# Kernel optimization log

Hardware: AMD Instinct MI355X
Metric: run time of the kernel (lower is better)

Reference implementation:

```python
import jax, jax.numpy as jnp
import numpy as np

NEG_SLOPE = 0.2
LN_EPS = 1e-6

B, L, D, H = 32, 512, 256, 4
N = B * L
E = 65536
C = D  # per-head out channels (GATConv out_channels=d_model)


def setup_inputs() -> dict:
    key = jax.random.key(0)
    ks = jax.random.split(key, 10)
    s = 1.0 / np.sqrt(D)
    inputs = jax.random.normal(ks[0], (B, L, D), dtype=jnp.float32)
    edge_index = jax.random.randint(ks[1], (2, E), 0, N, dtype=jnp.int64)
    return {
        "inputs": inputs,
        "edge_index": edge_index,
        "ln_gamma": jnp.ones((D,), jnp.float32),
        "ln_beta": jnp.zeros((D,), jnp.float32),
        "W1": jax.random.normal(ks[2], (D, D), jnp.float32) * s,   # linear_before_gnn
        "b1": jnp.zeros((D,), jnp.float32),
        "W_gat": jax.random.normal(ks[3], (H * C, D), jnp.float32) * s,  # GATConv.lin (no bias)
        "att_src": jax.random.normal(ks[4], (H, C), jnp.float32) * s,
        "att_dst": jax.random.normal(ks[5], (H, C), jnp.float32) * s,
        "bias_gat": jnp.zeros((C,), jnp.float32),  # concat=False -> size out_channels
        "W2": jax.random.normal(ks[6], (D, D), jnp.float32) * s,   # linear_after_gnn
        "b2": jnp.zeros((D,), jnp.float32),
    }


def _gat_conv(x, edge_index, W_gat, att_src, att_dst, bias_gat):
    # x: [N, D] -> project to [N, H, C]
    xh = (x @ W_gat.T).reshape(N, H, C)
    # add self loops (PyG default add_self_loops=True)
    loops = jnp.arange(N, dtype=edge_index.dtype)
    src = jnp.concatenate([edge_index[0], loops])  # message source j
    dst = jnp.concatenate([edge_index[1], loops])  # message target i
    # per-node attention logits [N, H]
    a_src = jnp.einsum("nhc,hc->nh", xh, att_src)
    a_dst = jnp.einsum("nhc,hc->nh", xh, att_dst)
    # per-edge logits and segment softmax over destination node
    e = jax.nn.leaky_relu(a_src[src] + a_dst[dst], NEG_SLOPE)  # [Etot, H]
    e_max = jax.ops.segment_max(e, dst, num_segments=N)        # every node has a self loop
    e = jnp.exp(e - e_max[dst])
    denom = jax.ops.segment_sum(e, dst, num_segments=N)
    alpha = e / denom[dst]                                     # [Etot, H]
    # weighted message aggregation (dropout on alpha skipped: eval mode)
    msg = xh[src] * alpha[:, :, None]                          # [Etot, H, C]
    out = jax.ops.segment_sum(msg, dst, num_segments=N)        # [N, H, C]
    return out.mean(axis=1) + bias_gat                         # concat=False -> head mean


def reference(inputs, edge_index, ln_gamma, ln_beta, W1, b1, W_gat, att_src, att_dst, bias_gat, W2, b2):
    # LayerNorm(eps=1e-6)
    mu = inputs.mean(-1, keepdims=True)
    var = jnp.mean((inputs - mu) ** 2, axis=-1, keepdims=True)
    x = (inputs - mu) * jax.lax.rsqrt(var + LN_EPS) * ln_gamma + ln_beta
    x = x.reshape(-1, D)
    gnn_in = x @ W1.T + b1
    gnn_out = _gat_conv(gnn_in, edge_index, W_gat, att_src, att_dst, bias_gat)
    y = gnn_out @ W2.T + b2
    # dropout is identity in eval mode; residual add
    return y.reshape(B, L, D) + inputs
```

## Files before the change

### kernel.cpp

```cpp
#include <hip/hip_runtime.h>
#include <math.h>

#define N_NODES 16384
#define D_MODEL 256
#define H_HEADS 4
#define C_CH 256
#define E_EDGES 65536
#define ETOT (E_EDGES + N_NODES)
#define HC 1024
#define MAXDEG 64
#define PSZ 262144

typedef __bf16 bf16x8 __attribute__((ext_vector_type(8)));
typedef __bf16 bf16x4 __attribute__((ext_vector_type(4)));
typedef float f32x4 __attribute__((ext_vector_type(4)));

__device__ __forceinline__ __bf16 f2bf(float f) { return (__bf16)f; }
__device__ __forceinline__ float bf2f(__bf16 b) { return (float)b; }

__global__ __launch_bounds__(256) void prep1_ln(
    const float* __restrict__ Wg, const float* __restrict__ att_src,
    const float* __restrict__ att_dst, const float* __restrict__ W2,
    const int* __restrict__ ei, const float* __restrict__ in,
    const float* __restrict__ gamma, const float* __restrict__ beta,
    float* __restrict__ t, float* __restrict__ Vp, int* __restrict__ cnt,
    int* __restrict__ csr, __bf16* __restrict__ x_ln)
{
    int b = blockIdx.x;
    int tid = threadIdx.x;
    if (b >= 1408) {
        int wave = tid >> 6, lane = tid & 63;
        int row = (b - 1408) * 4 + wave;
        float4 v = ((const float4*)(in + (size_t)row * D_MODEL))[lane];
        float s  = v.x + v.y + v.z + v.w;
        float sq = v.x*v.x + v.y*v.y + v.z*v.z + v.w*v.w;
        for (int off = 32; off; off >>= 1) {
            s  += __shfl_xor(s,  off);
            sq += __shfl_xor(sq, off);
        }
        float mean = s * (1.0f / D_MODEL);
        float var  = sq * (1.0f / D_MODEL) - mean * mean;
        float inv  = rsqrtf(var + 1e-6f);
        float4 g = ((const float4*)gamma)[lane];
        float4 bb = ((const float4*)beta)[lane];
        bf16x4 o;
        o[0] = f2bf((v.x - mean) * inv * g.x + bb.x);
        o[1] = f2bf((v.y - mean) * inv * g.y + bb.y);
        o[2] = f2bf((v.z - mean) * inv * g.z + bb.z);
        o[3] = f2bf((v.w - mean) * inv * g.w + bb.w);
        *(bf16x4*)(x_ln + (size_t)row * D_MODEL + lane * 4) = o;
        return;
    }
    if (b < 64) {
        int v = b >> 3, sl = b & 7, h = v & 3;
        const float* att = ((v < 4) ? att_src : att_dst) + h * C_CH;
        float acc = 0.f;
        #pragma unroll
        for (int j = 0; j < 32; ++j) {
            int c = sl * 32 + j;
            acc = fmaf(Wg[(size_t)(h * 256 + c) * 256 + tid], att[c], acc);
        }
        atomicAdd(&t[v * 256 + tid], acc);
        return;
    }
    if (b < 1088) {
        int bb2 = b - 64;
        int orig = bb2 >> 2, cs = bb2 & 3;
        int og = (orig & 63) * 4, h = orig >> 6;
        const float* w2r = W2 + (size_t)og * 256;
        const float* wgp = Wg + ((size_t)h * 256) * 256 + tid;
        float a0 = 0.f, a1 = 0.f, a2 = 0.f, a3 = 0.f;
        int cb = cs * 64;
        #pragma unroll 4
        for (int c = cb; c < cb + 64; ++c) {
            float wv = wgp[(size_t)c * 256];
            a0 = fmaf(w2r[c],       wv, a0);
            a1 = fmaf(w2r[256 + c], wv, a1);
            a2 = fmaf(w2r[512 + c], wv, a2);
            a3 = fmaf(w2r[768 + c], wv, a3);
        }
        size_t base = (size_t)cs * PSZ + (size_t)og * 1024 + h * 256 + tid;
        Vp[base]        = a0;
        Vp[base + 1024] = a1;
        Vp[base + 2048] = a2;
        Vp[base + 3072] = a3;
        return;
    }
    {
        int e = (b - 1088) * 256 + tid;
        int src, dst;
        if (e < E_EDGES) { src = ei[e]; dst = ei[E_EDGES + e]; }
        else             { src = dst = e - E_EDGES; }
        int pos = atomicAdd(cnt + dst, 1);
        csr[(size_t)dst * MAXDEG + pos] = src;
    }
}

__global__ __launch_bounds__(256) void prep2(
    const float* __restrict__ t, const float* __restrict__ W1,
    const float* __restrict__ b1, const float* __restrict__ Vp,
    const float* __restrict__ W2, const float* __restrict__ bg,
    const float* __restrict__ b2, float* __restrict__ u2,
    float* __restrict__ c0, float* __restrict__ Wzp,
    float* __restrict__ bias_z)
{
    __shared__ float red[4][4];
    __shared__ float vsh[4][64];
    int b = blockIdx.x;
    int d = threadIdx.x;

    if (b < 1024) {
        int orig = b >> 2, ks = b & 3;
        int og = (orig & 63) * 4, h = orig >> 6;
        int lane = d & 63, wid = d >> 6;
        int kb = ks * 64;
        size_t vbase = (size_t)og * 1024 + h * 256;

        {
            int j = d >> 6, kk = d & 63;
            float s = 0.f;
            #pragma unroll
            for (int cs = 0; cs < 4; ++cs)
                s += Vp[(size_t)cs * PSZ + vbase + (size_t)j * 1024 + kb + kk];
            vsh[j][kk] = s;
        }
        __syncthreads();

        float a0 = 0.f, a1 = 0.f, a2 = 0.f, a3 = 0.f;
        #pragma unroll 4
        for (int k = 0; k < 64; ++k) {
            float w1v = W1[(size_t)(kb + k) * 256 + d];
            a0 = fmaf(vsh[0][k], w1v, a0);
            a1 = fmaf(vsh[1][k], w1v, a1);
            a2 = fmaf(vsh[2][k], w1v, a2);
            a3 = fmaf(vsh[3][k], w1v, a3);
        }
        size_t base = (size_t)ks * PSZ + vbase + d;
        Wzp[base]        = a0;
        Wzp[base + 1024] = a1;
        Wzp[base + 2048] = a2;
        Wzp[base + 3072] = a3;

        if (ks == 0) {
            float b1v = b1[d];
            #pragma unroll
            for (int j = 0; j < 4; ++j) {
                float vsum = 0.f;
                #pragma unroll
                for (int cs = 0; cs < 4; ++cs)
                    vsum += Vp[(size_t)cs * PSZ + vbase + (size_t)j * 1024 + d];
                float p = vsum * b1v;
                for (int s = 32; s; s >>= 1) p += __shfl_xor(p, s);
                if (lane == 0) red[j][wid] = p;
            }
            __syncthreads();
            if (d < 4) {
                float s = red[d][0] + red[d][1] + red[d][2] + red[d][3];
                atomicAdd(&bias_z[og + d], 0.25f * s);
            }
            if (h == 0) {
                __syncthreads();
                float bgv = bg[d];
                #pragma unroll
                for (int j = 0; j < 4; ++j) {
                    float q = W2[(size_t)(og + j) * 256 + d] * bgv;
                    for (int s = 32; s; s >>= 1) q += __shfl_xor(q, s);
                    if (lane == 0) red[j][wid] = q;
                }
                __syncthreads();
                if (d < 4) {
                    float s = red[d][0] + red[d][1] + red[d][2] + red[d][3];
                    atomicAdd(&bias_z[og + d], s + b2[og + d]);
                }
            }
        }
        return;
    }
    {
        int bb = b - 1024;
        int v = bb >> 3, sl = bb & 7;
        const float* tv = t + v * 256;
        float acc = 0.f;
        #pragma unroll
        for (int j = 0; j < 32; ++j) {
            int k = sl * 32 + j;
            acc = fmaf(tv[k], W1[(size_t)k * 256 + d], acc);
        }
        atomicAdd(&u2[v * 256 + d], acc);
        if (d < 32) {
            float p = tv[sl * 32 + d] * b1[sl * 32 + d];
            for (int s = 16; s; s >>= 1) p += __shfl_xor(p, s);
            if (d == 0) atomicAdd(&c0[v], p);
        }
    }
}

__global__ __launch_bounds__(256) void logits_cvt(
    const __bf16* __restrict__ x_ln, const float* __restrict__ u2,
    const float* __restrict__ c0, float* __restrict__ a_src,
    float* __restrict__ a_dst, const float* __restrict__ Wzp,
    __bf16* __restrict__ Wz)
{
    int b = blockIdx.x;
    int tid = threadIdx.x;
    if (b >= 4096) {
        int idx = (b - 4096) * 256 + tid;
        float4 v = make_float4(0.f, 0.f, 0.f, 0.f);
        #pragma unroll
        for (int p = 0; p < 4; ++p) {
            float4 t4 = ((const float4*)(Wzp + (size_t)p * PSZ))[idx];
            v.x += t4.x; v.y += t4.y; v.z += t4.z; v.w += t4.w;
        }
        bf16x4 o;
        o[0] = f2bf(v.x); o[1] = f2bf(v.y); o[2] = f2bf(v.z); o[3] = f2bf(v.w);
        *(bf16x4*)(Wz + (size_t)idx * 4) = o;
        return;
    }
    __shared__ float u2s[8][256];
    __shared__ float c0s[8];
    #pragma unroll
    for (int k = 0; k < 8; ++k) u2s[k][tid] = u2[k * 256 + tid];
    if (tid < 8) c0s[tid] = c0[tid];
    __syncthreads();

    int wave = tid >> 6, lane = tid & 63;
    int n = b * 4 + wave;
    int v = lane >> 3, p = lane & 7;
    const __bf16* xp = x_ln + (size_t)n * D_MODEL + p * 32;
    const float*  up = &u2s[v][p * 32];
    float acc = 0.f;
    #pragma unroll
    for (int ti = 0; ti < 4; ++ti) {
        bf16x8 x = *(const bf16x8*)(xp + ti * 8);
        #pragma unroll
        for (int j = 0; j < 8; ++j)
            acc = fmaf(bf2f(x[j]), up[ti * 8 + j], acc);
    }
    acc += __shfl_xor(acc, 1);
    acc += __shfl_xor(acc, 2);
    acc += __shfl_xor(acc, 4);
    if (p == 0) {
        float o = acc + c0s[v];
        if (v < 4) a_src[n * H_HEADS + v] = o;
        else       a_dst[n * H_HEADS + (v - 4)] = o;
    }
}

#define TPAD 1032

__global__ __launch_bounds__(512, 1) void gat_gemm(
    const __bf16* __restrict__ x_ln, const float* __restrict__ a_src,
    const float* __restrict__ a_dst, const int* __restrict__ cnt,
    const int* __restrict__ csr, const __bf16* __restrict__ Wz,
    const float* __restrict__ bias_z, const float* __restrict__ resid,
    float* __restrict__ outf)
{
    __shared__ __align__(16) __bf16 T[64 * TPAD];
    int tid = threadIdx.x;
    int lane = tid & 63, w = tid >> 6;
    int m0 = blockIdx.x * 64;

    #pragma unroll 2
    for (int nn = 0; nn < 8; ++nn) {
        int node = w * 8 + nn;
        int i = m0 + node;
        int deg = cnt[i];
        int sidx = csr[(size_t)i * MAXDEG + lane];
        float4 ad = *(const float4*)(a_dst + i * H_HEADS);

        float4 wgt = make_float4(0.f, 0.f, 0.f, 0.f);
        if (lane < deg) {
            float4 as = *(const float4*)(a_src + sidx * H_HEADS);
            float l0 = as.x + ad.x, l1 = as.y + ad.y,
                  l2 = as.z + ad.z, l3 = as.w + ad.w;
            l0 = (l0 > 0.f) ? l0 : 0.2f * l0;
            l1 = (l1 > 0.f) ? l1 : 0.2f * l1;
            l2 = (l2 > 0.f) ? l2 : 0.2f * l2;
            l3 = (l3 > 0.f) ? l3 : 0.2f * l3;
            wgt = make_float4(__expf(l0), __expf(l1), __expf(l2), __expf(l3));
        }
        float s0 = wgt.x, s1 = wgt.y, s2 = wgt.z, s3 = wgt.w;
        #pragma unroll
        for (int off = 32; off; off >>= 1) {
            s0 += __shfl_xor(s0, off);
            s1 += __shfl_xor(s1, off);
            s2 += __shfl_xor(s2, off);
            s3 += __shfl_xor(s3, off);
        }

        float acc[4][4] = {};
        for (int e0 = 0; e0 < deg; e0 += 8) {
            bf16x4 X[8];
            float4 W[8];
            #pragma unroll
            for (int j = 0; j < 8; ++j) {
                int ee = e0 + j;
                bool val = ee < deg;
                int el = val ? ee : 0;
                int s = __shfl(sidx, el);
                X[j] = *(const bf16x4*)(x_ln + (size_t)s * D_MODEL + lane * 4);
                float4 wv;
                wv.x = __shfl(wgt.x, el);
                wv.y = __shfl(wgt.y, el);
                wv.z = __shfl(wgt.z, el);
                wv.w = __shfl(wgt.w, el);
                W[j] = val ? wv : make_float4(0.f, 0.f, 0.f, 0.f);
            }
            #pragma unroll
            for (int j = 0; j < 8; ++j) {
                #pragma unroll
                for (int d = 0; d < 4; ++d) {
                    float xv = bf2f(X[j][d]);
                    acc[0][d] = fmaf(W[j].x, xv, acc[0][d]);
                    acc[1][d] = fmaf(W[j].y, xv, acc[1][d]);
                    acc[2][d] = fmaf(W[j].z, xv, acc[2][d]);
                    acc[3][d] = fmaf(W[j].w, xv, acc[3][d]);
                }
            }
        }
        float sc[4] = {0.25f / s0, 0.25f / s1, 0.25f / s2, 0.25f / s3};
        #pragma unroll
        for (int h = 0; h < 4; ++h) {
            bf16x4 o;
            #pragma unroll
            for (int j = 0; j < 4; ++j) o[j] = f2bf(acc[h][j] * sc[h]);
            *(bf16x4*)(T + node * TPAD + h * 256 + lane * 4) = o;
        }
    }
    __syncthreads();

    int quad = lane >> 4, l16 = lane & 15;
    int n0 = w * 32;
    f32x4 pacc[4][2] = {};
    #pragma unroll 4
    for (int kk = 0; kk < HC; kk += 32) {
        bf16x8 af[4], bfr[2];
        #pragma unroll
        for (int mt = 0; mt < 4; ++mt)
            af[mt] = *(const bf16x8*)(T + (mt * 16 + l16) * TPAD
                                      + kk + quad * 8);
        #pragma unroll
        for (int nt = 0; nt < 2; ++nt)
            bfr[nt] = *(const bf16x8*)(Wz + (size_t)(n0 + nt * 16 + l16) * HC
                                       + kk + quad * 8);
        #pragma unroll
        for (int mt = 0; mt < 4; ++mt)
            #pragma unroll
            for (int nt = 0; nt < 2; ++nt)
                pacc[mt][nt] = __builtin_amdgcn_mfma_f32_16x16x32_bf16(
                    af[mt], bfr[nt], pacc[mt][nt], 0, 0, 0);
    }

    #pragma unroll
    for (int nt = 0; nt < 2; ++nt) {
        int col = n0 + nt * 16 + l16;
        float bv = bias_z[col];
        #pragma unroll
        for (int mt = 0; mt < 4; ++mt) {
            int row = m0 + mt * 16 + quad * 4;
            #pragma unroll
            for (int r = 0; r < 4; ++r) {
                size_t off = (size_t)(row + r) * C_CH + col;
                outf[off] = pacc[mt][nt][r] + bv + resid[off];
            }
        }
    }
}

extern "C" void kernel_launch(void* const* d_in, const int* in_sizes, int n_in,
                              void* d_out, int out_size, void* d_ws, size_t ws_size,
                              hipStream_t stream)
{
    const float* inp      = (const float*)d_in[0];
    const int*   ei       = (const int*)  d_in[1];
    const float* ln_gamma = (const float*)d_in[2];
    const float* ln_beta  = (const float*)d_in[3];
    const float* W1       = (const float*)d_in[4];
    const float* b1       = (const float*)d_in[5];
    const float* W_gat    = (const float*)d_in[6];
    const float* att_src  = (const float*)d_in[7];
    const float* att_dst  = (const float*)d_in[8];
    const float* bias_gat = (const float*)d_in[9];
    const float* W2       = (const float*)d_in[10];
    const float* b2       = (const float*)d_in[11];

    char* ws = (char*)d_ws;
    __bf16* x_ln_bf = (__bf16*)(ws);
    __bf16* Wz_b    = (__bf16*)(ws + (40ull << 20));
    float*  a_src_b = (float*)(ws + (41ull << 20));
    float*  a_dst_b = a_src_b + (size_t)N_NODES * H_HEADS;
    float*  t_vec   = (float*)(ws + (42ull << 20));
    float*  u2      = t_vec + 2048;
    float*  c0      = u2 + 2048;
    float*  bias_z  = c0 + 8;
    int*    cnt     = (int*)(bias_z + 256);
    int*    csr     = (int*)(ws + (45ull << 20));
    float*  Vp      = (float*)(ws + (49ull << 20));
    float*  Wzp     = (float*)(ws + (57ull << 20));

    size_t zbytes = (2048 + 2048 + 8 + 256) * sizeof(float)
                  + N_NODES * sizeof(int);
    hipMemsetAsync(t_vec, 0, zbytes, stream);

    prep1_ln<<<1408 + 4096, 256, 0, stream>>>(W_gat, att_src, att_dst, W2, ei,
                                              inp, ln_gamma, ln_beta,
                                              t_vec, Vp, cnt, csr, x_ln_bf);
    prep2<<<1088, 256, 0, stream>>>(t_vec, W1, b1, Vp, W2, bias_gat, b2,
                                    u2, c0, Wzp, bias_z);
    logits_cvt<<<4096 + 256, 256, 0, stream>>>(x_ln_bf, u2, c0,
                                               a_src_b, a_dst_b, Wzp, Wz_b);
    gat_gemm<<<N_NODES / 64, 512, 0, stream>>>(x_ln_bf, a_src_b, a_dst_b,
                                               cnt, csr, Wz_b, bias_z,
                                               inp, (float*)d_out);
}
```

Baseline: 154.5 us.

## Halve gat_gemm row tile to 32 nodes and prefetch Wz fragments

```diff
diff --git a/kernel.cpp b/kernel.cpp
--- a/kernel.cpp
+++ b/kernel.cpp
@@ -248,21 +248,21 @@
 
 #define TPAD 1032
 
-__global__ __launch_bounds__(512, 1) void gat_gemm(
+__global__ __launch_bounds__(512, 4) void gat_gemm(
     const __bf16* __restrict__ x_ln, const float* __restrict__ a_src,
     const float* __restrict__ a_dst, const int* __restrict__ cnt,
     const int* __restrict__ csr, const __bf16* __restrict__ Wz,
     const float* __restrict__ bias_z, const float* __restrict__ resid,
     float* __restrict__ outf)
 {
-    __shared__ __align__(16) __bf16 T[64 * TPAD];
+    __shared__ __align__(16) __bf16 T[32 * TPAD];
     int tid = threadIdx.x;
     int lane = tid & 63, w = tid >> 6;
-    int m0 = blockIdx.x * 64;
+    int m0 = blockIdx.x * 32;
 
     #pragma unroll 2
-    for (int nn = 0; nn < 8; ++nn) {
-        int node = w * 8 + nn;
+    for (int nn = 0; nn < 4; ++nn) {
+        int node = w * 4 + nn;
         int i = m0 + node;
         int deg = cnt[i];
         int sidx = csr[(size_t)i * MAXDEG + lane];
@@ -331,24 +331,24 @@
 
     int quad = lane >> 4, l16 = lane & 15;
     int n0 = w * 32;
-    f32x4 pacc[4][2] = {};
+    f32x4 pacc[2][2] = {};
+    const __bf16* wzr0 = Wz + (size_t)(n0 + l16) * HC + quad * 8;
+    const __bf16* wzr1 = Wz + (size_t)(n0 + 16 + l16) * HC + quad * 8;
+    bf16x8 bn0 = *(const bf16x8*)(wzr0);
+    bf16x8 bn1 = *(const bf16x8*)(wzr1);
     #pragma unroll 4
     for (int kk = 0; kk < HC; kk += 32) {
-        bf16x8 af[4], bfr[2];
-        #pragma unroll
-        for (int mt = 0; mt < 4; ++mt)
-            af[mt] = *(const bf16x8*)(T + (mt * 16 + l16) * TPAD
-                                      + kk + quad * 8);
-        #pragma unroll
-        for (int nt = 0; nt < 2; ++nt)
-            bfr[nt] = *(const bf16x8*)(Wz + (size_t)(n0 + nt * 16 + l16) * HC
-                                       + kk + quad * 8);
-        #pragma unroll
-        for (int mt = 0; mt < 4; ++mt)
-            #pragma unroll
-            for (int nt = 0; nt < 2; ++nt)
-                pacc[mt][nt] = __builtin_amdgcn_mfma_f32_16x16x32_bf16(
-                    af[mt], bfr[nt], pacc[mt][nt], 0, 0, 0);
+        bf16x8 bc0 = bn0, bc1 = bn1;
+        if (kk + 32 < HC) {
+            bn0 = *(const bf16x8*)(wzr0 + kk + 32);
+            bn1 = *(const bf16x8*)(wzr1 + kk + 32);
+        }
+        bf16x8 af0 = *(const bf16x8*)(T + l16 * TPAD + kk + quad * 8);
+        bf16x8 af1 = *(const bf16x8*)(T + (16 + l16) * TPAD + kk + quad * 8);
+        pacc[0][0] = __builtin_amdgcn_mfma_f32_16x16x32_bf16(af0, bc0, pacc[0][0], 0, 0, 0);
+        pacc[0][1] = __builtin_amdgcn_mfma_f32_16x16x32_bf16(af0, bc1, pacc[0][1], 0, 0, 0);
+        pacc[1][0] = __builtin_amdgcn_mfma_f32_16x16x32_bf16(af1, bc0, pacc[1][0], 0, 0, 0);
+        pacc[1][1] = __builtin_amdgcn_mfma_f32_16x16x32_bf16(af1, bc1, pacc[1][1], 0, 0, 0);
     }
 
     #pragma unroll
@@ -356,7 +356,7 @@
         int col = n0 + nt * 16 + l16;
         float bv = bias_z[col];
         #pragma unroll
-        for (int mt = 0; mt < 4; ++mt) {
+        for (int mt = 0; mt < 2; ++mt) {
             int row = m0 + mt * 16 + quad * 4;
             #pragma unroll
             for (int r = 0; r < 4; ++r) {
@@ -409,7 +409,7 @@
                                     u2, c0, Wzp, bias_z);
     logits_cvt<<<4096 + 256, 256, 0, stream>>>(x_ln_bf, u2, c0,
                                                a_src_b, a_dst_b, Wzp, Wz_b);
-    gat_gemm<<<N_NODES / 64, 512, 0, stream>>>(x_ln_bf, a_src_b, a_dst_b,
+    gat_gemm<<<N_NODES / 32, 512, 0, stream>>>(x_ln_bf, a_src_b, a_dst_b,
                                                cnt, csr, Wz_b, bias_z,
                                                inp, (float*)d_out);
 }
```

Measured after the change: 161.9 us. 4.8% more time.
